# Optimization experiments

Hardware: AMD Instinct MI355X
Metric: run time of the kernel (lower is better)

## Reference

```python
import jax, jax.numpy as jnp
import numpy as np


def _binarize(w):
    # adaptive per-output-channel scale: alpha = mean(|w|) over input dim (detached)
    alpha = jax.lax.stop_gradient(jnp.mean(jnp.abs(w), axis=1, keepdims=True))
    bw = alpha * jnp.sign(w)
    # straight-through estimator: forward uses bw, backward passes grad to w
    return w + jax.lax.stop_gradient(bw - w)


def setup_inputs() -> dict:
    key = jax.random.key(0)
    k1, k2, k3, k4, k5 = jax.random.split(key, 5)
    D, H = 1024, 4096
    x = jax.random.normal(k1, (64, 196, D), dtype=jnp.float32)
    w1 = jax.random.normal(k2, (H, D), dtype=jnp.float32) * 0.02
    b1 = jax.random.normal(k3, (H,), dtype=jnp.float32) * 0.02
    w2 = jax.random.normal(k4, (D, H), dtype=jnp.float32) * 0.02
    b2 = jax.random.normal(k5, (D,), dtype=jnp.float32) * 0.02
    return {"x": x, "w1": w1, "b1": b1, "w2": w2, "b2": b2}


def reference(x, w1, b1, w2, b2):
    # fc1: binary-weight linear -> GELU (exact, erf) -> fc2: binary-weight linear
    # dropout prob = 0.0 -> identity
    bw1 = _binarize(w1)  # [H, D]
    h = jnp.einsum('bsd,hd->bsh', x, bw1) + b1  # [B, S, H]
    h = jax.nn.gelu(h, approximate=False)
    bw2 = _binarize(w2)  # [D, H]
    out = jnp.einsum('bsh,dh->bsd', h, bw2) + b2  # [B, S, D]
    return out
```

## Files before the change

kernel.cpp:

```cpp
#include <hip/hip_runtime.h>
#include <hip/hip_bf16.h>
#include <cstdint>
#include <cstddef>

typedef __bf16 bf16x8 __attribute__((ext_vector_type(8)));
typedef float f32x4 __attribute__((ext_vector_type(4)));

#define AS1(p) ((const __attribute__((address_space(1))) void*)(p))
#define AS3(p) ((__attribute__((address_space(3))) void*)(p))

__device__ __forceinline__ unsigned short f2bf_rne(float f) {
    union { float f; unsigned u; } c; c.f = f;
    unsigned u = c.u;
    unsigned r = (u + 0x7FFFu + ((u >> 16) & 1u)) >> 16;
    return (unsigned short)r;
}

__global__ __launch_bounds__(256)
void binarize_k(const float* __restrict__ W, unsigned short* __restrict__ Sg,
                float* __restrict__ Alpha, int C) {
    const int r = blockIdx.x;
    const float4* w = (const float4*)(W + (size_t)r * C);
    ushort4* s = (ushort4*)(Sg + (size_t)r * C);
    const int n4 = C >> 2;
    float lsum = 0.f;
    for (int i = threadIdx.x; i < n4; i += 256) {
        float4 v = w[i];
        lsum += fabsf(v.x) + fabsf(v.y) + fabsf(v.z) + fabsf(v.w);
        ushort4 o;
        o.x = (v.x == 0.f) ? 0 : ((v.x < 0.f) ? 0xBF80 : 0x3F80);
        o.y = (v.y == 0.f) ? 0 : ((v.y < 0.f) ? 0xBF80 : 0x3F80);
        o.z = (v.z == 0.f) ? 0 : ((v.z < 0.f) ? 0xBF80 : 0x3F80);
        o.w = (v.w == 0.f) ? 0 : ((v.w < 0.f) ? 0xBF80 : 0x3F80);
        s[i] = o;
    }
    for (int o = 32; o > 0; o >>= 1) lsum += __shfl_down(lsum, o, 64);
    __shared__ float red[4];
    const int lane = threadIdx.x & 63, wid = threadIdx.x >> 6;
    if (lane == 0) red[wid] = lsum;
    __syncthreads();
    if (threadIdx.x == 0) Alpha[r] = (red[0] + red[1] + red[2] + red[3]) / (float)C;
}

__global__ __launch_bounds__(256)
void f32_to_bf16_k(const float* __restrict__ X, unsigned short* __restrict__ Y, int n4) {
    const int stride = gridDim.x * 256;
    for (int i = blockIdx.x * 256 + threadIdx.x; i < n4; i += stride) {
        float4 v = ((const float4*)X)[i];
        ushort4 o;
        o.x = f2bf_rne(v.x); o.y = f2bf_rne(v.y);
        o.z = f2bf_rne(v.z); o.w = f2bf_rne(v.w);
        ((ushort4*)Y)[i] = o;
    }
}

template<int GELU>
__global__ __launch_bounds__(256, 2)
void gemm_bin(const unsigned short* __restrict__ A,
              const unsigned short* __restrict__ S,
              const float* __restrict__ alpha,
              const float* __restrict__ bias,
              unsigned short* __restrict__ Obf,
              float* __restrict__ Of32,
              int M, int N, int K)
{
    __shared__ unsigned short As[128][64];
    __shared__ unsigned short Ss[128][64];

    const int tid  = threadIdx.x;
    const int lane = tid & 63;
    const int wid  = tid >> 6;
    const int wr   = wid >> 1, wc = wid & 1;

    const int nbn = N >> 7;
    const int nbm = M >> 7;
    const int nwg = nbm * nbn;
    const int cpx = nwg >> 3;
    const int bid = blockIdx.x;
    const int swz = (bid & 7) * cpx + (bid >> 3);
    const int bm = swz / nbn;
    const int bn = swz % nbn;

    const unsigned short* gA = A + (size_t)bm * 128 * K;
    const unsigned short* gS = S + (size_t)bn * 128 * K;

    f32x4 acc[4][4] = {};
    const int lr = lane & 15;
    const int lk = (lane >> 4) * 8;

    const int nkt = K >> 6;
    for (int kt = 0; kt < nkt; ++kt) {
        const int k0 = kt << 6;
#pragma unroll
        for (int j = 0; j < 4; ++j) {
            const int idx = j * 256 + tid;
            const int r = idx >> 3;
            const int c = (idx & 7) * 8;
            __builtin_amdgcn_global_load_lds(AS1(gA + (size_t)r * K + k0 + c),
                                             AS3(&As[0][0] + idx * 8), 16, 0, 0);
            __builtin_amdgcn_global_load_lds(AS1(gS + (size_t)r * K + k0 + c),
                                             AS3(&Ss[0][0] + idx * 8), 16, 0, 0);
        }
        __syncthreads();

        bf16x8 af[2][4], bf[2][4];
#pragma unroll
        for (int ks = 0; ks < 2; ++ks) {
#pragma unroll
            for (int mf = 0; mf < 4; ++mf)
                af[ks][mf] = *(const bf16x8*)&As[wr * 64 + mf * 16 + lr][ks * 32 + lk];
#pragma unroll
            for (int nf = 0; nf < 4; ++nf)
                bf[ks][nf] = *(const bf16x8*)&Ss[wc * 64 + nf * 16 + lr][ks * 32 + lk];
        }
#pragma unroll
        for (int ks = 0; ks < 2; ++ks)
#pragma unroll
            for (int mf = 0; mf < 4; ++mf)
#pragma unroll
                for (int nf = 0; nf < 4; ++nf)
                    acc[mf][nf] = __builtin_amdgcn_mfma_f32_16x16x32_bf16(
                        af[ks][mf], bf[ks][nf], acc[mf][nf], 0, 0, 0);
        __syncthreads();
    }

    const int col0 = bn * 128 + wc * 64;
    const int row0 = bm * 128 + wr * 64;
    float al[4], bi[4];
#pragma unroll
    for (int nf = 0; nf < 4; ++nf) {
        const int n = col0 + nf * 16 + lr;
        al[nf] = alpha[n];
        bi[nf] = bias[n];
    }
#pragma unroll
    for (int mf = 0; mf < 4; ++mf) {
#pragma unroll
        for (int j = 0; j < 4; ++j) {
            const int m = row0 + mf * 16 + (lane >> 4) * 4 + j;
#pragma unroll
            for (int nf = 0; nf < 4; ++nf) {
                const int n = col0 + nf * 16 + lr;
                float v = acc[mf][nf][j] * al[nf] + bi[nf];
                if (GELU) {
                    v = 0.5f * v * (1.0f + erff(v * 0.70710678118654752f));
                    Obf[(size_t)m * N + n] = f2bf_rne(v);
                } else {
                    Of32[(size_t)m * N + n] = v;
                }
            }
        }
    }
}

extern "C" void kernel_launch(void* const* d_in, const int* in_sizes, int n_in,
                              void* d_out, int out_size, void* d_ws, size_t ws_size,
                              hipStream_t stream) {
    const float* x  = (const float*)d_in[0];
    const float* w1 = (const float*)d_in[1];
    const float* b1 = (const float*)d_in[2];
    const float* w2 = (const float*)d_in[3];
    const float* b2 = (const float*)d_in[4];
    float* out = (float*)d_out;

    const int D = 1024, H = 4096;
    const int M = in_sizes[0] / D;

    char* ws = (char*)d_ws;
    size_t off = 0;
    auto alloc = [&](size_t bytes) -> void* {
        void* p = ws + off;
        off = (off + bytes + 255) & ~(size_t)255;
        return p;
    };
    unsigned short* xb = (unsigned short*)alloc((size_t)M * D * 2);
    unsigned short* s1 = (unsigned short*)alloc((size_t)H * D * 2);
    float*          a1 = (float*)alloc((size_t)H * 4);
    unsigned short* s2 = (unsigned short*)alloc((size_t)D * H * 2);
    float*          a2 = (float*)alloc((size_t)D * 4);
    unsigned short* hb = (unsigned short*)alloc((size_t)M * H * 2);

    binarize_k<<<H, 256, 0, stream>>>(w1, s1, a1, D);
    binarize_k<<<D, 256, 0, stream>>>(w2, s2, a2, H);
    f32_to_bf16_k<<<2048, 256, 0, stream>>>(x, xb, (M * D) / 4);

    gemm_bin<1><<<(M / 128) * (H / 128), 256, 0, stream>>>(xb, s1, a1, b1, hb, nullptr, M, H, D);
    gemm_bin<0><<<(M / 128) * (D / 128), 256, 0, stream>>>(hb, s2, a2, b2, nullptr, out, M, D, H);
}
```

Baseline: 460.4 us.

## Rewrite binary GEMM as 256x256 double-buffered 8-wave pipelined kernel

Replaces the 128x128 single-buffered GEMM with a 256x256-tile, 512-thread kernel. It double-buffers LDS (128 KB), XOR-swizzles LDS columns to avoid bank conflicts, and interleaves global->LDS staging with MFMA quadrants using barriers and s_setprio. It also adds a remainder-aware XCD-aware block remap. The goal is to hide global load latency and raise arithmetic intensity, at the cost of higher register and LDS pressure. M=12544 is divisible by 256, so tiles cover it exactly.

```diff
diff --git a/kernel.cpp b/kernel.cpp
--- a/kernel.cpp
+++ b/kernel.cpp
@@ -55,77 +55,131 @@
 }
 
 template<int GELU>
-__global__ __launch_bounds__(256, 2)
-void gemm_bin(const unsigned short* __restrict__ A,
-              const unsigned short* __restrict__ S,
-              const float* __restrict__ alpha,
-              const float* __restrict__ bias,
-              unsigned short* __restrict__ Obf,
-              float* __restrict__ Of32,
-              int M, int N, int K)
+__global__ __launch_bounds__(512, 2)
+void gemm_bin8(const unsigned short* __restrict__ A,
+               const unsigned short* __restrict__ S,
+               const float* __restrict__ alpha,
+               const float* __restrict__ bias,
+               unsigned short* __restrict__ Obf,
+               float* __restrict__ Of32,
+               int M, int N, int K)
 {
-    __shared__ unsigned short As[128][64];
-    __shared__ unsigned short Ss[128][64];
+    __shared__ __align__(16) unsigned short lds[2][2][2][128 * 64];
 
     const int tid  = threadIdx.x;
     const int lane = tid & 63;
     const int wid  = tid >> 6;
-    const int wr   = wid >> 1, wc = wid & 1;
-
-    const int nbn = N >> 7;
-    const int nbm = M >> 7;
+    const int wr   = wid >> 2;
+    const int wc   = wid & 3;
+    const int lr   = lane & 15;
+    const int hi   = lane >> 4;
+    const int xorv = lr & 7;
+
+    const int nbn = N >> 8, nbm = M >> 8;
     const int nwg = nbm * nbn;
-    const int cpx = nwg >> 3;
-    const int bid = blockIdx.x;
-    const int swz = (bid & 7) * cpx + (bid >> 3);
-    const int bm = swz / nbn;
-    const int bn = swz % nbn;
-
-    const unsigned short* gA = A + (size_t)bm * 128 * K;
-    const unsigned short* gS = S + (size_t)bn * 128 * K;
-
-    f32x4 acc[4][4] = {};
-    const int lr = lane & 15;
-    const int lk = (lane >> 4) * 8;
-
-    const int nkt = K >> 6;
-    for (int kt = 0; kt < nkt; ++kt) {
-        const int k0 = kt << 6;
-#pragma unroll
-        for (int j = 0; j < 4; ++j) {
-            const int idx = j * 256 + tid;
-            const int r = idx >> 3;
-            const int c = (idx & 7) * 8;
-            __builtin_amdgcn_global_load_lds(AS1(gA + (size_t)r * K + k0 + c),
-                                             AS3(&As[0][0] + idx * 8), 16, 0, 0);
-            __builtin_amdgcn_global_load_lds(AS1(gS + (size_t)r * K + k0 + c),
-                                             AS3(&Ss[0][0] + idx * 8), 16, 0, 0);
-        }
-        __syncthreads();
-
-        bf16x8 af[2][4], bf[2][4];
-#pragma unroll
-        for (int ks = 0; ks < 2; ++ks) {
-#pragma unroll
-            for (int mf = 0; mf < 4; ++mf)
-                af[ks][mf] = *(const bf16x8*)&As[wr * 64 + mf * 16 + lr][ks * 32 + lk];
-#pragma unroll
-            for (int nf = 0; nf < 4; ++nf)
-                bf[ks][nf] = *(const bf16x8*)&Ss[wc * 64 + nf * 16 + lr][ks * 32 + lk];
-        }
-#pragma unroll
-        for (int ks = 0; ks < 2; ++ks)
-#pragma unroll
-            for (int mf = 0; mf < 4; ++mf)
-#pragma unroll
-                for (int nf = 0; nf < 4; ++nf)
-                    acc[mf][nf] = __builtin_amdgcn_mfma_f32_16x16x32_bf16(
-                        af[ks][mf], bf[ks][nf], acc[mf][nf], 0, 0, 0);
-        __syncthreads();
-    }
-
-    const int col0 = bn * 128 + wc * 64;
-    const int row0 = bm * 128 + wr * 64;
+    const int q = nwg >> 3, r = nwg & 7;
+    const int xcd = blockIdx.x & 7, loc = blockIdx.x >> 3;
+    const int swz = (xcd < r ? xcd * (q + 1) : r * (q + 1) + (xcd - r) * q) + loc;
+    const int bm = swz / nbn, bn = swz % nbn;
+
+    const unsigned short* gA = A + (size_t)bm * 256 * K;
+    const unsigned short* gB = S + (size_t)bn * 256 * K;
+
+    const unsigned short* Ab[2] = { &lds[0][0][wr][0], &lds[1][0][wr][0] };
+    const unsigned short* Bb[2] = { &lds[0][1][wc >> 1][0], &lds[1][1][wc >> 1][0] };
+    const int brow = (wc & 1) * 64;
+
+    f32x4 acc[8][4] = {};
+    bf16x8 af[2][4], bq0[2][2], bq1[2][2];
+
+    const int T = K >> 6;
+    const int niter = T >> 1;
+
+#define STAGE(BUF_, MAT_, HALF_, TILE_, GSRC_) do {                                   \
+    const unsigned short* _g = (GSRC_) + (size_t)(HALF_) * 128 * K + ((TILE_) << 6);  \
+    unsigned short* _l = &lds[BUF_][MAT_][HALF_][0];                                  \
+    _Pragma("unroll")                                                                 \
+    for (int _rd = 0; _rd < 2; ++_rd) {                                               \
+        const int _u = _rd * 512 + tid;                                               \
+        const int _row = _u >> 3;                                                     \
+        const int _sc = ((_u & 7) ^ (_row & 7)) << 3;                                 \
+        __builtin_amdgcn_global_load_lds(AS1(_g + (size_t)_row * K + _sc),            \
+                                         AS3(_l + _u * 8), 16, 0, 0);                 \
+    }                                                                                 \
+} while (0)
+
+#define LOAD_AF(BUF_, MB_) do {                                                       \
+    _Pragma("unroll")                                                                 \
+    for (int _ks = 0; _ks < 2; ++_ks)                                                 \
+    _Pragma("unroll")                                                                 \
+    for (int _mf = 0; _mf < 4; ++_mf)                                                 \
+        af[_ks][_mf] = *(const bf16x8*)(Ab[BUF_] + (((MB_)*4 + _mf) * 16 + lr) * 64   \
+                                        + (((_ks << 2) + hi) ^ xorv) * 8);            \
+} while (0)
+
+#define LOAD_BF(ARR_, BUF_, NB_) do {                                                 \
+    _Pragma("unroll")                                                                 \
+    for (int _ks = 0; _ks < 2; ++_ks)                                                 \
+    _Pragma("unroll")                                                                 \
+    for (int _nf = 0; _nf < 2; ++_nf)                                                 \
+        ARR_[_ks][_nf] = *(const bf16x8*)(Bb[BUF_] + (brow + ((NB_)*2 + _nf) * 16 + lr) * 64 \
+                                          + (((_ks << 2) + hi) ^ xorv) * 8);          \
+} while (0)
+
+#define MFMA_Q(MB_, ARR_, NB_) do {                                                   \
+    _Pragma("unroll")                                                                 \
+    for (int _ks = 0; _ks < 2; ++_ks)                                                 \
+    _Pragma("unroll")                                                                 \
+    for (int _mf = 0; _mf < 4; ++_mf)                                                 \
+    _Pragma("unroll")                                                                 \
+    for (int _nf = 0; _nf < 2; ++_nf)                                                 \
+        acc[(MB_)*4 + _mf][(NB_)*2 + _nf] = __builtin_amdgcn_mfma_f32_16x16x32_bf16(  \
+            af[_ks][_mf], ARR_[_ks][_nf], acc[(MB_)*4 + _mf][(NB_)*2 + _nf], 0, 0, 0);\
+} while (0)
+
+#define BAR() __builtin_amdgcn_s_barrier()
+#define VMW4() asm volatile("s_waitcnt vmcnt(4)" ::: "memory")
+
+    STAGE(0, 1, 0, 0, gB); STAGE(0, 1, 1, 0, gB);
+    STAGE(0, 0, 0, 0, gA); STAGE(0, 0, 1, 0, gA);
+    STAGE(1, 1, 0, 1, gB); STAGE(1, 1, 1, 1, gB);
+    VMW4();
+    BAR();
+
+    for (int i = 0; i < niter; ++i) {
+        const int t  = 2 * i;
+        const int t1 = t + 1;
+        const int t2 = (t + 2 < T) ? t + 2 : 0;
+        const int t3 = (t + 3 < T) ? t + 3 : 1;
+
+        LOAD_AF(0, 0); LOAD_BF(bq0, 0, 0);
+        STAGE(1, 0, 0, t1, gA);
+        BAR(); __builtin_amdgcn_s_setprio(1); MFMA_Q(0, bq0, 0); __builtin_amdgcn_s_setprio(0); BAR();
+        LOAD_BF(bq1, 0, 1);
+        STAGE(1, 0, 1, t1, gA);
+        BAR(); __builtin_amdgcn_s_setprio(1); MFMA_Q(0, bq1, 1); __builtin_amdgcn_s_setprio(0); BAR();
+        LOAD_AF(0, 1);
+        STAGE(0, 1, 0, t2, gB);
+        BAR(); __builtin_amdgcn_s_setprio(1); MFMA_Q(1, bq0, 0); __builtin_amdgcn_s_setprio(0); BAR();
+        STAGE(0, 1, 1, t2, gB);
+        BAR(); __builtin_amdgcn_s_setprio(1); MFMA_Q(1, bq1, 1); __builtin_amdgcn_s_setprio(0);
+        VMW4(); BAR();
+        LOAD_AF(1, 0); LOAD_BF(bq0, 1, 0);
+        STAGE(0, 0, 0, t2, gA);
+        BAR(); __builtin_amdgcn_s_setprio(1); MFMA_Q(0, bq0, 0); __builtin_amdgcn_s_setprio(0); BAR();
+        LOAD_BF(bq1, 1, 1);
+        STAGE(0, 0, 1, t2, gA);
+        BAR(); __builtin_amdgcn_s_setprio(1); MFMA_Q(0, bq1, 1); __builtin_amdgcn_s_setprio(0); BAR();
+        LOAD_AF(1, 1);
+        STAGE(1, 1, 0, t3, gB);
+        BAR(); __builtin_amdgcn_s_setprio(1); MFMA_Q(1, bq0, 0); __builtin_amdgcn_s_setprio(0); BAR();
+        STAGE(1, 1, 1, t3, gB);
+        BAR(); __builtin_amdgcn_s_setprio(1); MFMA_Q(1, bq1, 1); __builtin_amdgcn_s_setprio(0);
+        VMW4(); BAR();
+    }
+
+    const int col0 = bn * 256 + wc * 64;
+    const int row0 = bm * 256 + wr * 128;
     float al[4], bi[4];
 #pragma unroll
     for (int nf = 0; nf < 4; ++nf) {
@@ -134,10 +188,10 @@
         bi[nf] = bias[n];
     }
 #pragma unroll
-    for (int mf = 0; mf < 4; ++mf) {
+    for (int mf = 0; mf < 8; ++mf) {
 #pragma unroll
         for (int j = 0; j < 4; ++j) {
-            const int m = row0 + mf * 16 + (lane >> 4) * 4 + j;
+            const int m = row0 + mf * 16 + hi * 4 + j;
 #pragma unroll
             for (int nf = 0; nf < 4; ++nf) {
                 const int n = col0 + nf * 16 + lr;
@@ -151,6 +205,12 @@
             }
         }
     }
+#undef STAGE
+#undef LOAD_AF
+#undef LOAD_BF
+#undef MFMA_Q
+#undef BAR
+#undef VMW4
 }
 
 extern "C" void kernel_launch(void* const* d_in, const int* in_sizes, int n_in,
@@ -184,6 +244,6 @@
     binarize_k<<<D, 256, 0, stream>>>(w2, s2, a2, H);
     f32_to_bf16_k<<<2048, 256, 0, stream>>>(x, xb, (M * D) / 4);
 
-    gemm_bin<1><<<(M / 128) * (H / 128), 256, 0, stream>>>(xb, s1, a1, b1, hb, nullptr, M, H, D);
-    gemm_bin<0><<<(M / 128) * (D / 128), 256, 0, stream>>>(hb, s2, a2, b2, nullptr, out, M, D, H);
-}
+    gemm_bin8<1><<<(M / 256) * (H / 256), 512, 0, stream>>>(xb, s1, a1, b1, hb, nullptr, M, H, D);
+    gemm_bin8<0><<<(M / 256) * (D / 256), 512, 0, stream>>>(hb, s2, a2, b2, nullptr, out, M, D, H);
+}
```

After: 393.9 us. -14.4%, faster.

## Add XOR-swizzled LDS layout, templated N tile, and remainder-safe XCD swizzle

Applied to the files above, without the earlier changes.

The LDS tiles are now stored with an XOR swizzle on the 16-byte column chunk, applied in both the global-to-LDS copy and the fragment reads, to cut bank conflicts on the bf16x8 loads. The GEMM is templated on the N tile width; the second GEMM (N=1024, K=4096) uses a 64-wide tile so more workgroups fill the CUs. The XCD block remap now handles workgroup counts not divisible by 8, and the min-blocks-per-CU launch bound is dropped. The narrower tile lowers B reuse per A load and raises A traffic for fc2.

```diff
diff --git a/kernel.cpp b/kernel.cpp
--- a/kernel.cpp
+++ b/kernel.cpp
@@ -54,8 +54,8 @@
     }
 }
 
-template<int GELU>
-__global__ __launch_bounds__(256, 2)
+template<int GELU, int BN>
+__global__ __launch_bounds__(256)
 void gemm_bin(const unsigned short* __restrict__ A,
               const unsigned short* __restrict__ S,
               const float* __restrict__ alpha,
@@ -64,71 +64,82 @@
               float* __restrict__ Of32,
               int M, int N, int K)
 {
-    __shared__ unsigned short As[128][64];
-    __shared__ unsigned short Ss[128][64];
+    constexpr int NF = BN / 64;
+    constexpr int WN = BN / 2;
+    constexpr int NFRAG = WN / 16;
+    (void)sizeof(char[NF > 0 ? 1 : 1]);
+
+    __shared__ __align__(16) unsigned short As[128 * 64];
+    __shared__ __align__(16) unsigned short Ss[BN * 64];
 
     const int tid  = threadIdx.x;
     const int lane = tid & 63;
     const int wid  = tid >> 6;
     const int wr   = wid >> 1, wc = wid & 1;
-
-    const int nbn = N >> 7;
-    const int nbm = M >> 7;
+    const int lr   = lane & 15;
+    const int hi   = lane >> 4;
+    const int xorv = lr & 7;
+
+    const int nbn = N / BN, nbm = M >> 7;
     const int nwg = nbm * nbn;
-    const int cpx = nwg >> 3;
-    const int bid = blockIdx.x;
-    const int swz = (bid & 7) * cpx + (bid >> 3);
-    const int bm = swz / nbn;
-    const int bn = swz % nbn;
+    const int q = nwg >> 3, r = nwg & 7;
+    const int xcd = blockIdx.x & 7, loc = blockIdx.x >> 3;
+    const int swz = (xcd < r ? xcd * (q + 1) : r * (q + 1) + (xcd - r) * q) + loc;
+    const int bm = swz / nbn, bn = swz % nbn;
 
     const unsigned short* gA = A + (size_t)bm * 128 * K;
-    const unsigned short* gS = S + (size_t)bn * 128 * K;
-
-    f32x4 acc[4][4] = {};
-    const int lr = lane & 15;
-    const int lk = (lane >> 4) * 8;
+    const unsigned short* gS = S + (size_t)bn * BN * K;
+
+    f32x4 acc[4][NFRAG] = {};
 
     const int nkt = K >> 6;
     for (int kt = 0; kt < nkt; ++kt) {
         const int k0 = kt << 6;
 #pragma unroll
         for (int j = 0; j < 4; ++j) {
-            const int idx = j * 256 + tid;
-            const int r = idx >> 3;
-            const int c = (idx & 7) * 8;
-            __builtin_amdgcn_global_load_lds(AS1(gA + (size_t)r * K + k0 + c),
-                                             AS3(&As[0][0] + idx * 8), 16, 0, 0);
-            __builtin_amdgcn_global_load_lds(AS1(gS + (size_t)r * K + k0 + c),
-                                             AS3(&Ss[0][0] + idx * 8), 16, 0, 0);
+            const int u = j * 256 + tid;
+            const int row = u >> 3;
+            const int sc = ((u & 7) ^ (row & 7)) << 3;
+            __builtin_amdgcn_global_load_lds(AS1(gA + (size_t)row * K + k0 + sc),
+                                             AS3(&As[0] + u * 8), 16, 0, 0);
+        }
+#pragma unroll
+        for (int j = 0; j < BN / 32; ++j) {
+            const int u = j * 256 + tid;
+            const int row = u >> 3;
+            const int sc = ((u & 7) ^ (row & 7)) << 3;
+            __builtin_amdgcn_global_load_lds(AS1(gS + (size_t)row * K + k0 + sc),
+                                             AS3(&Ss[0] + u * 8), 16, 0, 0);
         }
         __syncthreads();
 
-        bf16x8 af[2][4], bf[2][4];
+        bf16x8 af[2][4], bf[2][NFRAG];
 #pragma unroll
         for (int ks = 0; ks < 2; ++ks) {
+            const int kg = ((ks << 2) + hi) ^ xorv;
 #pragma unroll
             for (int mf = 0; mf < 4; ++mf)
-                af[ks][mf] = *(const bf16x8*)&As[wr * 64 + mf * 16 + lr][ks * 32 + lk];
-#pragma unroll
-            for (int nf = 0; nf < 4; ++nf)
-                bf[ks][nf] = *(const bf16x8*)&Ss[wc * 64 + nf * 16 + lr][ks * 32 + lk];
+                af[ks][mf] = *(const bf16x8*)(&As[0] + (wr * 64 + mf * 16 + lr) * 64 + kg * 8);
+#pragma unroll
+            for (int nf = 0; nf < NFRAG; ++nf)
+                bf[ks][nf] = *(const bf16x8*)(&Ss[0] + (wc * WN + nf * 16 + lr) * 64 + kg * 8);
         }
 #pragma unroll
         for (int ks = 0; ks < 2; ++ks)
 #pragma unroll
             for (int mf = 0; mf < 4; ++mf)
 #pragma unroll
-                for (int nf = 0; nf < 4; ++nf)
+                for (int nf = 0; nf < NFRAG; ++nf)
                     acc[mf][nf] = __builtin_amdgcn_mfma_f32_16x16x32_bf16(
                         af[ks][mf], bf[ks][nf], acc[mf][nf], 0, 0, 0);
         __syncthreads();
     }
 
-    const int col0 = bn * 128 + wc * 64;
+    const int col0 = bn * BN + wc * WN;
     const int row0 = bm * 128 + wr * 64;
-    float al[4], bi[4];
-#pragma unroll
-    for (int nf = 0; nf < 4; ++nf) {
+    float al[NFRAG], bi[NFRAG];
+#pragma unroll
+    for (int nf = 0; nf < NFRAG; ++nf) {
         const int n = col0 + nf * 16 + lr;
         al[nf] = alpha[n];
         bi[nf] = bias[n];
@@ -137,9 +148,9 @@
     for (int mf = 0; mf < 4; ++mf) {
 #pragma unroll
         for (int j = 0; j < 4; ++j) {
-            const int m = row0 + mf * 16 + (lane >> 4) * 4 + j;
-#pragma unroll
-            for (int nf = 0; nf < 4; ++nf) {
+            const int m = row0 + mf * 16 + hi * 4 + j;
+#pragma unroll
+            for (int nf = 0; nf < NFRAG; ++nf) {
                 const int n = col0 + nf * 16 + lr;
                 float v = acc[mf][nf][j] * al[nf] + bi[nf];
                 if (GELU) {
@@ -184,6 +195,6 @@
     binarize_k<<<D, 256, 0, stream>>>(w2, s2, a2, H);
     f32_to_bf16_k<<<2048, 256, 0, stream>>>(x, xb, (M * D) / 4);
 
-    gemm_bin<1><<<(M / 128) * (H / 128), 256, 0, stream>>>(xb, s1, a1, b1, hb, nullptr, M, H, D);
-    gemm_bin<0><<<(M / 128) * (D / 128), 256, 0, stream>>>(hb, s2, a2, b2, nullptr, out, M, D, H);
-}
+    gemm_bin<1, 128><<<(M / 128) * (H / 128), 256, 0, stream>>>(xb, s1, a1, b1, hb, nullptr, M, H, D);
+    gemm_bin<0, 64><<<(M / 128) * (D / 64), 256, 0, stream>>>(hb, s2, a2, b2, nullptr, out, M, D, H);
+}
```

After: 403.8 us. 1.14x faster.
